# Kernel tuning notes

Hardware: AMD Instinct MI355X
Metric: run time of the kernel (lower is better)

## Reference

```python
import jax, jax.numpy as jnp
import numpy as np

N = 100_000          # nodes
E = 1_600_000        # edges
ORIG = 92            # orig_atom_fea_len
NBR = 41             # nbr_fea_len (RBF bins)
ATOM = 64            # atom_fea_len
NCONV = 3
H = 128              # h_fea_len
OUT = 1
NGRAPH = 256         # graphs in batch
ZDIM = 2 * ATOM + NBR  # CGConv concat dim = 169
RBF_VMIN, RBF_VMAX = 0.0, 8.0


def setup_inputs() -> dict:
    key = jax.random.key(0)
    ks = jax.random.split(key, 12)
    s = lambda fan: float(1.0 / np.sqrt(fan))
    u = lambda k, shape, fan: jax.random.uniform(k, shape, jnp.float32, -s(fan), s(fan))
    return {
        "x": jax.random.normal(ks[0], (N, ORIG), jnp.float32),
        "edge_attr": jax.random.normal(ks[1], (E, 3), jnp.float32),
        "W_emb": u(ks[2], (ORIG, ATOM), ORIG),
        "b_emb": u(ks[3], (ATOM,), ORIG),
        "Wf": u(ks[4], (NCONV, ZDIM, ATOM), ZDIM),
        "bf": u(ks[5], (NCONV, ATOM), ZDIM),
        "Ws": u(ks[6], (NCONV, ZDIM, ATOM), ZDIM),
        "bs": u(ks[7], (NCONV, ATOM), ZDIM),
        "bn_gamma": jnp.ones((NCONV, ATOM), jnp.float32),
        "bn_beta": jnp.zeros((NCONV, ATOM), jnp.float32),
        "W1": u(ks[8], (ATOM, H), ATOM),
        "b1": u(ks[9], (H,), ATOM),
        "W2": u(ks[10], (H, OUT), H),
        "b2": u(ks[11], (OUT,), H),
        "edge_index": jax.random.randint(jax.random.fold_in(key, 100), (2, E), 0, N),
        "batch": jnp.sort(jax.random.randint(jax.random.fold_in(key, 101), (N,), 0, NGRAPH)),
    }


def reference(x, edge_attr, W_emb, b_emb, Wf, bf, Ws, bs, bn_gamma, bn_beta,
              W1, b1, W2, b2, edge_index, batch):
    # atom embedding
    h = x @ W_emb + b_emb                                  # [N, ATOM]
    # edge distance -> RBF expansion (vmin=0, vmax=8, bins=NBR)
    d = jnp.sqrt(jnp.sum(edge_attr * edge_attr, axis=-1))  # [E]
    centers = jnp.linspace(RBF_VMIN, RBF_VMAX, NBR)
    gamma_rbf = 1.0 / ((RBF_VMAX - RBF_VMIN) / (NBR - 1))  # 1/lengthscale
    e = jnp.exp(-gamma_rbf * (d[:, None] - centers) ** 2)  # [E, NBR]

    src, dst = edge_index[0], edge_index[1]  # flow source->target: x_j = h[src], x_i = h[dst]
    for l in range(NCONV):
        # CGConv message: z = [x_i || x_j || e]; gate * core, scatter-add to i
        z = jnp.concatenate([h[dst], h[src], e], axis=-1)       # [E, ZDIM]
        msg = jax.nn.sigmoid(z @ Wf[l] + bf[l]) * jax.nn.softplus(z @ Ws[l] + bs[l])
        agg = jax.ops.segment_sum(msg, dst, num_segments=N)     # [N, ATOM]
        # BatchNorm (training-mode batch stats, eps=1e-5) then residual
        mu = agg.mean(axis=0)
        var = agg.var(axis=0)
        agg = bn_gamma[l] * (agg - mu) / jnp.sqrt(var + 1e-5) + bn_beta[l]
        h = jax.nn.softplus(agg + h)
    # global_add_pool over graphs, then MLP head
    g = jax.ops.segment_sum(h, batch, num_segments=NGRAPH)      # [NGRAPH, ATOM]
    out = jax.nn.softplus(g @ W1 + b1) @ W2 + b2                # [NGRAPH, OUT]
    return out
```

## Files before the change

kernel.cpp:

```cpp
#include <hip/hip_runtime.h>
#include <hip/hip_bf16.h>
#include <math.h>

#define N_NODES 100000
#define N_EDGES 1600000
#define ORIG    92
#define NBR     41
#define ATOM    64
#define NCONV   3
#define HFEA    128
#define NGRAPH  256
#define ZD      169
#define TBINS   5120
#define TMAX    10.0f
#define TS      ((TBINS + 1) * 64)
#define SP      72
#define SPE     136
#define NPBLK   128
#define LOG2E   1.4426950408889634f
#define LN2     0.6931471805599453f
#define NBKT    391
#define S1E     6250
#define S3CH    4096

typedef __attribute__((ext_vector_type(8))) short short8;
typedef __attribute__((ext_vector_type(4))) float f32x4;
typedef __attribute__((ext_vector_type(8))) int int8v;

__device__ __forceinline__ float softplus_f(float x) {
    return fmaxf(x, 0.0f) + log1pf(expf(-fabsf(x)));
}
__device__ __forceinline__ float sp_fast2(float x) {
    float t = x * LOG2E;
    return LN2 * (fmaxf(t, 0.0f) +
                  __builtin_amdgcn_logf(1.0f + __builtin_amdgcn_exp2f(-fabsf(t))));
}
__device__ __forceinline__ unsigned int pk_bf16(float lo, float hi) {
    unsigned int r;
    asm("v_cvt_pk_bf16_f32 %0, %1, %2" : "=v"(r) : "v"(lo), "v"(hi));
    return r;
}
__device__ __forceinline__ float bf_lo(unsigned int p) { return __uint_as_float(p << 16); }
__device__ __forceinline__ float bf_hi(unsigned int p) { return __uint_as_float(p & 0xffff0000u); }

__device__ __forceinline__ int lower_bound_i(const int* __restrict__ a, int n, int key) {
    int lo = 0, hi = n;
    while (lo < hi) {
        int mid = (lo + hi) >> 1;
        if (a[mid] < key) lo = mid + 1; else hi = mid;
    }
    return lo;
}

__global__ __launch_bounds__(256) void k_bhist(const int* __restrict__ ei,
                                               int* __restrict__ bucketCnt,
                                               int* __restrict__ flag,
                                               int* __restrict__ bucketBase,
                                               int* __restrict__ bucketCursor,
                                               int* __restrict__ offs) {
    __shared__ int cntL[NBKT];
    __shared__ int lastFlag;
    int tid = threadIdx.x;
    for (int i = tid; i < NBKT; i += 256) cntL[i] = 0;
    __syncthreads();
    int base = blockIdx.x * S1E;
    for (int i = tid; i < S1E; i += 256)
        atomicAdd(&cntL[ei[N_EDGES + base + i] >> 8], 1);
    __syncthreads();
    for (int i = tid; i < NBKT; i += 256)
        if (cntL[i]) atomicAdd(&bucketCnt[i], cntL[i]);
    if (tid == 0) {
        __threadfence();
        lastFlag = (atomicAdd(flag, 1) == 255) ? 1 : 0;
    }
    __syncthreads();
    if (lastFlag && tid < 64) {
        __threadfence();
        int carry = 0;
        for (int b0 = 0; b0 < NBKT; b0 += 64) {
            int idx = b0 + tid;
            int v0 = (idx < NBKT) ? bucketCnt[idx] : 0;
            int v = v0;
            for (int d = 1; d < 64; d <<= 1) {
                int u = __shfl_up(v, d, 64);
                if (tid >= d) v += u;
            }
            if (idx < NBKT) {
                int ex = carry + v - v0;
                bucketBase[idx] = ex;
                bucketCursor[idx] = ex;
            }
            carry += __shfl(v, 63, 64);
        }
        if (tid == 0) {
            bucketBase[NBKT] = N_EDGES;
            offs[N_NODES] = N_EDGES;
        }
    }
}

__global__ __launch_bounds__(256) void k_psort1(const int* __restrict__ ei,
                                                const float* __restrict__ ea,
                                                int* __restrict__ bucketCursor,
                                                int2* __restrict__ staging) {
    __shared__ int cntL[NBKT], scanB[NBKT], curL[NBKT], gbaseL[NBKT];
    __shared__ int sortedD[S3CH], sortedN[S3CH];
    int tid = threadIdx.x;
    int base = blockIdx.x * S3CH;
    int myCount = N_EDGES - base;
    if (myCount > S3CH) myCount = S3CH;
    for (int i = tid; i < NBKT; i += 256) { cntL[i] = 0; curL[i] = 0; }
    __syncthreads();
    int descr[16], dstr[16];
#pragma unroll
    for (int j = 0; j < 16; ++j) {
        int i = j * 256 + tid;
        descr[j] = 0; dstr[j] = -1;
        if (i < myCount) {
            int e = base + i;
            int src = ei[e];
            int dst = ei[N_EDGES + e];
            float a = ea[3 * e], bb = ea[3 * e + 1], c = ea[3 * e + 2];
            float d = sqrtf(a * a + bb * bb + c * c);
            int bin = (int)fminf(fmaf(d, (float)TBINS / TMAX, 0.5f), (float)TBINS);
            descr[j] = (bin << 17) | src;
            dstr[j] = dst;
            atomicAdd(&cntL[dst >> 8], 1);
        }
    }
    __syncthreads();
    if (tid < 64) {
        int carry = 0;
        for (int b0 = 0; b0 < NBKT; b0 += 64) {
            int idx = b0 + tid;
            int v0 = (idx < NBKT) ? cntL[idx] : 0;
            int v = v0;
            for (int d = 1; d < 64; d <<= 1) {
                int u = __shfl_up(v, d, 64);
                if (tid >= d) v += u;
            }
            if (idx < NBKT) scanB[idx] = carry + v - v0;
            carry += __shfl(v, 63, 64);
        }
    }
    __syncthreads();
#pragma unroll
    for (int j = 0; j < 16; ++j) {
        if (dstr[j] >= 0) {
            int b = dstr[j] >> 8;
            int pos = scanB[b] + atomicAdd(&curL[b], 1);
            sortedD[pos] = descr[j];
            sortedN[pos] = dstr[j];
        }
    }
    for (int i = tid; i < NBKT; i += 256)
        if (cntL[i] > 0) gbaseL[i] = atomicAdd(&bucketCursor[i], cntL[i]);
    __syncthreads();
    for (int i = tid; i < myCount; i += 256) {
        int n = sortedN[i];
        int b = n >> 8;
        int2 pr; pr.x = sortedD[i]; pr.y = n;
        staging[gbaseL[b] + (i - scanB[b])] = pr;
    }
}

__global__ __launch_bounds__(256) void k_psort2(const int* __restrict__ bucketBase,
                                                const int2* __restrict__ staging,
                                                int* __restrict__ edesc,
                                                int* __restrict__ offs) {
    __shared__ int cnt[256], sbase[256], cur[256];
    int b = blockIdx.x, tid = threadIdx.x;
    int base = bucketBase[b];
    int nb = bucketBase[b + 1] - base;
    cnt[tid] = 0; cur[tid] = 0;
    __syncthreads();
    for (int i = tid; i < nb; i += 256)
        atomicAdd(&cnt[staging[base + i].y & 255], 1);
    __syncthreads();
    int v = cnt[tid];
    sbase[tid] = v;
    __syncthreads();
    for (int d = 1; d < 256; d <<= 1) {
        int u = (tid >= d) ? sbase[tid - d] : 0;
        __syncthreads();
        sbase[tid] += u;
        __syncthreads();
    }
    int ex = sbase[tid] - v;
    int dst = (b << 8) + tid;
    if (dst < N_NODES) offs[dst] = base + ex;
    sbase[tid] = ex;
    __syncthreads();
    for (int i = tid; i < nb; i += 256) {
        int2 pr = staging[base + i];
        int local = pr.y & 255;
        int pos = base + sbase[local] + atomicAdd(&cur[local], 1);
        edesc[pos] = pr.x;
    }
}

__global__ __launch_bounds__(256) void k_table2(const float* __restrict__ Wf,
                                                const float* __restrict__ bf,
                                                const float* __restrict__ Ws,
                                                const float* __restrict__ bs,
                                                const float* __restrict__ We,
                                                unsigned int* __restrict__ Tp,
                                                unsigned int* __restrict__ Bp,
                                                unsigned int* __restrict__ BpE) {
    int tid = threadIdx.x;
    int l = blockIdx.y;
    if (blockIdx.x == 161) {
        int m = tid >> 6, c = tid & 63;
        const float* Wb = ((m & 2) ? Ws : Wf) + (size_t)l * ZD * ATOM + (m & 1) * ATOM * ATOM + c;
        unsigned int* dst = Bp + (size_t)l * 8192 + (size_t)tid * 32;
        for (int kp = 0; kp < 32; ++kp) {
            float w0 = Wb[(2 * kp) * ATOM] * LOG2E;
            float w1 = Wb[(2 * kp + 1) * ATOM] * LOG2E;
            dst[kp] = pk_bf16(w0, w1);
        }
        return;
    }
    if (blockIdx.x == 162) {
        if (l != 0) return;
        int n = tid & 63, q = tid >> 6;
        for (int kp = q * 16; kp < q * 16 + 16; ++kp) {
            int k0 = 2 * kp, k1 = 2 * kp + 1;
            float w0 = (k0 < ORIG) ? We[k0 * ATOM + n] : 0.f;
            float w1 = (k1 < ORIG) ? We[k1 * ATOM + n] : 0.f;
            BpE[(size_t)n * 64 + kp] = pk_bf16(w0, w1);
        }
        return;
    }
    __shared__ float Wc[NBR * 64], Wsc[NBR * 64], R[32 * NBR];
    int b0 = blockIdx.x * 32;
    const float* srcf = Wf + (size_t)l * ZD * ATOM + 2 * ATOM * ATOM;
    const float* srcs = Ws + (size_t)l * ZD * ATOM + 2 * ATOM * ATOM;
    for (int i = tid; i < NBR * 64; i += 256) {
        Wc[i] = srcf[i] * LOG2E;
        Wsc[i] = srcs[i] * LOG2E;
    }
    for (int i = tid; i < 32 * NBR; i += 256) {
        int bin = i / NBR, k = i - bin * NBR;
        float d = (b0 + bin) * (TMAX / TBINS);
        float diff = d - 0.2f * k;
        R[i] = expf(-5.0f * diff * diff);
    }
    __syncthreads();
    int c = tid & 63;
    float afb = bf[l * ATOM + c] * LOG2E, asb = bs[l * ATOM + c] * LOG2E;
#pragma unroll
    for (int it = 0; it < 8; ++it) {
        int bin = (tid >> 6) + 4 * it;
        int gb = b0 + bin;
        if (gb <= TBINS) {
            float af = afb, as = asb;
            for (int k = 0; k < NBR; ++k) {
                float r = R[bin * NBR + k];
                af += r * Wc[k * 64 + c];
                as += r * Wsc[k * 64 + c];
            }
            Tp[(size_t)l * TS + (size_t)gb * 64 + c] = pk_bf16(af, as);
        }
    }
}

__global__ __launch_bounds__(256) void k_embed_nodeP(const float* __restrict__ x,
                                                     const unsigned int* __restrict__ BpE,
                                                     const float* __restrict__ be,
                                                     const unsigned int* __restrict__ Bp,
                                                     float* __restrict__ h,
                                                     unsigned int* __restrict__ Pi,
                                                     unsigned int* __restrict__ Pj) {
    __shared__ char smem[46080];
    short* Ae = (short*)smem;
    short* Be = (short*)(smem + 17408);
    short* Bn = (short*)smem;
    short* An = (short*)(smem + 36864);
    int tid = threadIdx.x;
    int n0 = blockIdx.x * 64;
    for (int i = tid; i < 64 * 64; i += 256) {
        int r = i >> 6, kp = i & 63;
        int node = n0 + r;
        float2 v = make_float2(0.f, 0.f);
        if (node < N_NODES && kp < 46) v = ((const float2*)x)[(size_t)node * 46 + kp];
        *(unsigned int*)&Ae[r * SPE + kp * 2] = pk_bf16(v.x, v.y);
    }
    {
        const uint4* src = (const uint4*)BpE;
        for (int i = tid; i < 64 * 16; i += 256) {
            int row = i >> 4, q = i & 15;
            *(uint4*)&Be[row * SPE + q * 8] = src[i];
        }
    }
    __syncthreads();
    int lane = tid & 63, w = tid >> 6;
    int c15 = lane & 15, kb = lane >> 4;
    {
        short8 af[4];
#pragma unroll
        for (int s = 0; s < 4; ++s)
            af[s] = *(const short8*)&Ae[(16 * w + c15) * SPE + s * 32 + kb * 8];
        f32x4 acc[4];
#pragma unroll
        for (int t = 0; t < 4; ++t) acc[t] = (f32x4){0.f, 0.f, 0.f, 0.f};
#pragma unroll
        for (int t = 0; t < 4; ++t) {
#pragma unroll
            for (int s = 0; s < 4; ++s) {
                short8 bf8 = *(const short8*)&Be[(16 * t + c15) * SPE + s * 32 + kb * 8];
                acc[t] = __builtin_amdgcn_mfma_f32_16x16x32_bf16(af[s], bf8, acc[t], 0, 0, 0);
            }
        }
#pragma unroll
        for (int t = 0; t < 4; ++t) {
            float bias = be[16 * t + c15];
#pragma unroll
            for (int reg = 0; reg < 4; ++reg) {
                int row = 16 * w + kb * 4 + reg;
                int node = n0 + row;
                float v = acc[t][reg] + bias;
                if (node < N_NODES) h[(size_t)node * 64 + 16 * t + c15] = v;
                An[row * SP + 16 * t + c15] = (short)pk_bf16(v, v);
            }
        }
    }
    __syncthreads();
    {
        const uint4* src = (const uint4*)Bp;
        for (int i = tid; i < 2048; i += 256) {
            int row = i >> 3, j = i & 7;
            *(uint4*)&Bn[row * SP + j * 8] = src[row * 8 + j];
        }
    }
    __syncthreads();
    short8 af2[2];
#pragma unroll
    for (int s = 0; s < 2; ++s)
        af2[s] = *(const short8*)&An[(16 * w + c15) * SP + s * 32 + kb * 8];
    f32x4 acc2[16];
#pragma unroll
    for (int t = 0; t < 16; ++t) acc2[t] = (f32x4){0.f, 0.f, 0.f, 0.f};
#pragma unroll
    for (int t = 0; t < 16; ++t) {
#pragma unroll
        for (int s = 0; s < 2; ++s) {
            short8 bf8 = *(const short8*)&Bn[(16 * t + c15) * SP + s * 32 + kb * 8];
            acc2[t] = __builtin_amdgcn_mfma_f32_16x16x32_bf16(af2[s], bf8, acc2[t], 0, 0, 0);
        }
    }
#pragma unroll
    for (int t = 0; t < 4; ++t) {
#pragma unroll
        for (int reg = 0; reg < 4; ++reg) {
            int row = kb * 4 + reg;
            int node = n0 + 16 * w + row;
            if (node < N_NODES) {
                Pi[(size_t)node * 64 + 16 * t + c15] = pk_bf16(acc2[t][reg], acc2[t + 8][reg]);
                Pj[(size_t)node * 64 + 16 * t + c15] = pk_bf16(acc2[t + 4][reg], acc2[t + 12][reg]);
            }
        }
    }
}

__global__ __launch_bounds__(256) void k_nodeP_mfma(float* __restrict__ h,
                                                    const float* __restrict__ agg,
                                                    const float* __restrict__ ss,
                                                    const unsigned int* __restrict__ Bp,
                                                    int l,
                                                    unsigned int* __restrict__ Pi,
                                                    unsigned int* __restrict__ Pj) {
    __shared__ short A[64 * SP];
    __shared__ short B[256 * SP];
    int tid = threadIdx.x;
    int n0 = blockIdx.x * 64;
    for (int i = tid; i < 64 * 32; i += 256) {
        int r = i >> 5, kp = i & 31;
        int node = n0 + r;
        int gi = node * 32 + kp;
        float2 hv = make_float2(0.f, 0.f);
        if (node < N_NODES) {
            hv = ((const float2*)h)[gi];
            float2 av = ((const float2*)agg)[gi];
            int c = kp * 2;
            float x0 = ss[c] * av.x + ss[64 + c] + hv.x;
            float x1 = ss[c + 1] * av.y + ss[64 + c + 1] + hv.y;
            hv.x = sp_fast2(x0);
            hv.y = sp_fast2(x1);
            ((float2*)h)[gi] = hv;
        }
        *(unsigned int*)&A[r * SP + kp * 2] = pk_bf16(hv.x, hv.y);
    }
    {
        const uint4* src = (const uint4*)(Bp + (size_t)l * 8192);
        for (int i = tid; i < 2048; i += 256) {
            int row = i >> 3, j = i & 7;
            *(uint4*)&B[row * SP + j * 8] = src[row * 8 + j];
        }
    }
    __syncthreads();
    int lane = tid & 63, w = tid >> 6;
    int c15 = lane & 15, kb = lane >> 4;
    short8 af[2];
#pragma unroll
    for (int s = 0; s < 2; ++s)
        af[s] = *(const short8*)&A[(16 * w + c15) * SP + s * 32 + kb * 8];
    f32x4 acc[16];
#pragma unroll
    for (int t = 0; t < 16; ++t) acc[t] = (f32x4){0.f, 0.f, 0.f, 0.f};
#pragma unroll
    for (int t = 0; t < 16; ++t) {
#pragma unroll
        for (int s = 0; s < 2; ++s) {
            short8 bf8 = *(const short8*)&B[(16 * t + c15) * SP + s * 32 + kb * 8];
            acc[t] = __builtin_amdgcn_mfma_f32_16x16x32_bf16(af[s], bf8, acc[t], 0, 0, 0);
        }
    }
#pragma unroll
    for (int t = 0; t < 4; ++t) {
#pragma unroll
        for (int reg = 0; reg < 4; ++reg) {
            int row = kb * 4 + reg;
            int node = n0 + 16 * w + row;
            if (node < N_NODES) {
                Pi[(size_t)node * 64 + 16 * t + c15] = pk_bf16(acc[t][reg], acc[t + 8][reg]);
                Pj[(size_t)node * 64 + 16 * t + c15] = pk_bf16(acc[t + 4][reg], acc[t + 12][reg]);
            }
        }
    }
}

__global__ __launch_bounds__(256, 4) void k_edge_sorted(const int* __restrict__ offs,
                                                        const int* __restrict__ edesc,
                                                        const unsigned int* __restrict__ Pi,
                                                        const unsigned int* __restrict__ Pj,
                                                        const unsigned int* __restrict__ Tp,
                                                        float* __restrict__ agg) {
    int wid = (blockIdx.x * 256 + threadIdx.x) >> 6;
    int lane = threadIdx.x & 63;
    if (wid >= N_NODES) return;
    int uwid = __builtin_amdgcn_readfirstlane(wid);
    int2 kk;
    asm volatile("s_load_dwordx2 %0, %1, 0x0\n\ts_waitcnt lgkmcnt(0)"
                 : "=s"(kk) : "s"(offs + uwid));
    int ko = kk.x, ke = kk.y;
    unsigned int pi = Pi[(size_t)uwid * 64 + lane];
    float gi = bf_lo(pi), ci = bf_hi(pi);
    float acc = 0.0f;
    int lane4 = lane * 4;
    const char* PjB = (const char*)Pj;
    const char* TpB = (const char*)Tp;
    int k0 = ko;
    for (; k0 + 16 <= ke; k0 += 16) {
        int8v e0, e1;
        asm volatile(
            "s_load_dwordx8 %0, %2, 0x0\n\t"
            "s_load_dwordx8 %1, %2, 0x20\n\t"
            "s_waitcnt lgkmcnt(0)"
            : "=&s"(e0), "=&s"(e1)
            : "s"(edesc + k0));
        unsigned int pjv[16], tjv[16];
#pragma unroll
        for (int j = 0; j < 16; ++j) {
            int v = (j < 8) ? e0[j & 7] : e1[j & 7];
            int sb = (v & 0x1FFFF) << 8;
            int tb = (v >> 17) << 8;
            pjv[j] = *(const unsigned int*)(PjB + sb + lane4);
            tjv[j] = *(const unsigned int*)(TpB + tb + lane4);
        }
#pragma unroll
        for (int j = 0; j < 16; ++j) {
            float g = gi + bf_lo(pjv[j]) + bf_lo(tjv[j]);
            float c = ci + bf_hi(pjv[j]) + bf_hi(tjv[j]);
            float sg = __builtin_amdgcn_rcpf(1.0f + __builtin_amdgcn_exp2f(-g));
            float sp = fmaxf(c, 0.0f) + __builtin_amdgcn_logf(1.0f + __builtin_amdgcn_exp2f(-fabsf(c)));
            acc = fmaf(sg, sp, acc);
        }
    }
    if (k0 < ke) {
        int8v e0, e1;
        asm volatile(
            "s_load_dwordx8 %0, %2, 0x0\n\t"
            "s_load_dwordx8 %1, %2, 0x20\n\t"
            "s_waitcnt lgkmcnt(0)"
            : "=&s"(e0), "=&s"(e1)
            : "s"(edesc + k0));
        unsigned int pjv[16], tjv[16];
#pragma unroll
        for (int j = 0; j < 16; ++j) {
            if (k0 + j < ke) {
                int v = (j < 8) ? e0[j & 7] : e1[j & 7];
                int sb = (v & 0x1FFFF) << 8;
                int tb = (v >> 17) << 8;
                pjv[j] = *(const unsigned int*)(PjB + sb + lane4);
                tjv[j] = *(const unsigned int*)(TpB + tb + lane4);
            }
        }
#pragma unroll
        for (int j = 0; j < 16; ++j) {
            if (k0 + j < ke) {
                float g = gi + bf_lo(pjv[j]) + bf_lo(tjv[j]);
                float c = ci + bf_hi(pjv[j]) + bf_hi(tjv[j]);
                float sg = __builtin_amdgcn_rcpf(1.0f + __builtin_amdgcn_exp2f(-g));
                float sp = fmaxf(c, 0.0f) + __builtin_amdgcn_logf(1.0f + __builtin_amdgcn_exp2f(-fabsf(c)));
                acc = fmaf(sg, sp, acc);
            }
        }
    }
    agg[(size_t)uwid * 64 + lane] = acc * LN2;
}

__global__ __launch_bounds__(256) void k_bnstats2(const float* __restrict__ agg,
                                                  float* __restrict__ partial,
                                                  int* __restrict__ lcnt,
                                                  const float* __restrict__ gamma,
                                                  const float* __restrict__ beta,
                                                  int l, float* __restrict__ ss) {
    __shared__ f32x4 ls4[256], ls24[256];
    __shared__ float ls[128];
    __shared__ int lastFlag;
    int tid = threadIdx.x;
    const f32x4* agg4 = (const f32x4*)agg;
    f32x4 s = (f32x4){0.f, 0.f, 0.f, 0.f};
    f32x4 s2 = (f32x4){0.f, 0.f, 0.f, 0.f};
    for (int i = blockIdx.x * 256 + tid; i < N_NODES * 16; i += NPBLK * 256) {
        f32x4 v = agg4[i];
        s += v;
        s2 += v * v;
    }
    ls4[tid] = s; ls24[tid] = s2;
    __syncthreads();
    for (int d = 128; d >= 16; d >>= 1) {
        if (tid < d) { ls4[tid] += ls4[tid + d]; ls24[tid] += ls24[tid + d]; }
        __syncthreads();
    }
    if (tid < 16) {
#pragma unroll
        for (int j = 0; j < 4; ++j) {
            partial[blockIdx.x * 128 + tid * 4 + j] = ls4[tid][j];
            partial[blockIdx.x * 128 + 64 + tid * 4 + j] = ls24[tid][j];
        }
    }
    __syncthreads();
    if (tid == 0) {
        __threadfence();
        lastFlag = (atomicAdd(lcnt, 1) == NPBLK - 1) ? 1 : 0;
    }
    __syncthreads();
    if (lastFlag) {
        __threadfence();
        if (tid < 128) {
            float sum = 0.0f;
            for (int b = 0; b < NPBLK; ++b) sum += partial[b * 128 + tid];
            ls[tid] = sum;
        }
        __syncthreads();
        if (tid < 64) {
            const float inv = 1.0f / (float)N_NODES;
            float mu = ls[tid] * inv;
            float var = ls[64 + tid] * inv - mu * mu;
            float sc = gamma[l * ATOM + tid] * rsqrtf(var + 1e-5f);
            ss[tid] = sc;
            ss[64 + tid] = beta[l * ATOM + tid] - mu * sc;
        }
    }
}

__global__ __launch_bounds__(128) void k_head2(const float* __restrict__ agg,
                                               const float* __restrict__ ss,
                                               const float* __restrict__ h,
                                               const int* __restrict__ batch,
                                               const float* __restrict__ W1,
                                               const float* __restrict__ b1,
                                               const float* __restrict__ W2,
                                               const float* __restrict__ b2,
                                               float* __restrict__ out) {
    __shared__ float gvec[64];
    __shared__ float red[128];
    int gid = blockIdx.x, tid = threadIdx.x;
    int lo = lower_bound_i(batch, N_NODES, gid);
    int hi = lower_bound_i(batch, N_NODES, gid + 1);
    int c = tid & 63, half = tid >> 6;
    float sc = ss[c], sh = ss[64 + c];
    float acc = 0.0f;
    for (int n = lo + half; n < hi; n += 2) {
        float xv = sc * agg[(size_t)n * 64 + c] + sh + h[(size_t)n * 64 + c];
        acc += sp_fast2(xv);
    }
    red[tid] = acc;
    __syncthreads();
    if (tid < 64) gvec[tid] = red[tid] + red[tid + 64];
    __syncthreads();
    float a2 = b1[tid];
    for (int k = 0; k < ATOM; ++k) a2 += gvec[k] * W1[k * HFEA + tid];
    red[tid] = softplus_f(a2) * W2[tid];
    __syncthreads();
    for (int s = 64; s > 0; s >>= 1) {
        if (tid < s) red[tid] += red[tid + s];
        __syncthreads();
    }
    if (tid == 0) out[gid] = red[0] + b2[0];
}

extern "C" void kernel_launch(void* const* d_in, const int* in_sizes, int n_in,
                              void* d_out, int out_size, void* d_ws, size_t ws_size,
                              hipStream_t stream) {
    const float* x       = (const float*)d_in[0];
    const float* ea      = (const float*)d_in[1];
    const float* W_emb   = (const float*)d_in[2];
    const float* b_emb   = (const float*)d_in[3];
    const float* Wf      = (const float*)d_in[4];
    const float* bf      = (const float*)d_in[5];
    const float* Ws      = (const float*)d_in[6];
    const float* bs      = (const float*)d_in[7];
    const float* bn_g    = (const float*)d_in[8];
    const float* bn_b    = (const float*)d_in[9];
    const float* W1      = (const float*)d_in[10];
    const float* b1      = (const float*)d_in[11];
    const float* W2      = (const float*)d_in[12];
    const float* b2      = (const float*)d_in[13];
    const int*   ei      = (const int*)d_in[14];
    const int*   batch   = (const int*)d_in[15];
    float* out = (float*)d_out;

    char* wsb = (char*)d_ws;
    size_t off = 0;
    auto alloc = [&](size_t bytes) { char* p = wsb + off; off += (bytes + 255) & ~(size_t)255; return p; };
    float*        h        = (float*)alloc((size_t)N_NODES * 64 * 4);
    float*        agg      = (float*)alloc((size_t)N_NODES * 64 * 4);
    unsigned int* Pi       = (unsigned int*)alloc((size_t)N_NODES * 64 * 4);
    unsigned int* Pj       = (unsigned int*)alloc((size_t)N_NODES * 64 * 4);
    int*          edesc    = (int*)alloc((size_t)(N_EDGES + 16) * 4);
    int2*         staging  = (int2*)alloc((size_t)N_EDGES * 8);
    int*          meta     = (int*)alloc(1024 * 4);
    int*          bucketCnt    = meta;
    int*          lcnt         = meta + 512;
    int*          bucketBase   = (int*)alloc(520 * 4);
    int*          bucketCursor = (int*)alloc(512 * 4);
    int*          offs     = (int*)alloc((size_t)(N_NODES + 1) * 4);
    unsigned int* Tp       = (unsigned int*)alloc((size_t)NCONV * TS * 4);
    unsigned int* Bp       = (unsigned int*)alloc((size_t)NCONV * 8192 * 4);
    unsigned int* BpE      = (unsigned int*)alloc((size_t)64 * 64 * 4);
    float*        partial  = (float*)alloc((size_t)NPBLK * 128 * 4);
    float*        ss       = (float*)alloc(128 * 4);

    (void)hipMemsetAsync(meta, 0, 1024 * 4, stream);
    k_bhist<<<256, 256, 0, stream>>>(ei, bucketCnt, lcnt + 3, bucketBase, bucketCursor, offs);
    k_psort1<<<(N_EDGES + S3CH - 1) / S3CH, 256, 0, stream>>>(ei, ea, bucketCursor, staging);
    k_psort2<<<NBKT, 256, 0, stream>>>(bucketBase, staging, edesc, offs);

    dim3 tg(163, NCONV);
    k_table2<<<tg, 256, 0, stream>>>(Wf, bf, Ws, bs, W_emb, Tp, Bp, BpE);
    k_embed_nodeP<<<(N_NODES + 63) / 64, 256, 0, stream>>>(x, BpE, b_emb, Bp, h, Pi, Pj);

    for (int l = 0; l < NCONV; ++l) {
        if (l > 0)
            k_nodeP_mfma<<<(N_NODES + 63) / 64, 256, 0, stream>>>(h, agg, ss, Bp, l, Pi, Pj);
        k_edge_sorted<<<(N_NODES * 64 + 255) / 256, 256, 0, stream>>>(
            offs, edesc, Pi, Pj, Tp + (size_t)l * TS, agg);
        k_bnstats2<<<NPBLK, 256, 0, stream>>>(agg, partial, lcnt + l, bn_g, bn_b, l, ss);
    }

    k_head2<<<NGRAPH, 128, 0, stream>>>(agg, ss, h, batch, W1, b1, W2, b2, out);
}
```

Baseline: 501.5 us.

## Split pooling into node-parallel atomic pool kernel and separate MLP head

Global add pooling used to run as one block per graph (256 blocks), each binary-searching the sorted batch array and looping over about 390 nodes with 128 threads. It is now a node-parallel kernel of about 1563 blocks in which each wavefront covers 16 consecutive nodes, keeps a running sum per graph and flushes it with atomicAdd whenever the graph id changes. A small separate head kernel then runs the MLP. The goal is better GPU occupancy for the final pooling pass, at the cost of an extra memset, an extra launch and float atomics, which make the summation order nondeterministic.

```diff
diff --git a/kernel.cpp b/kernel.cpp
--- a/kernel.cpp
+++ b/kernel.cpp
@@ -42,15 +42,6 @@
 }
 __device__ __forceinline__ float bf_lo(unsigned int p) { return __uint_as_float(p << 16); }
 __device__ __forceinline__ float bf_hi(unsigned int p) { return __uint_as_float(p & 0xffff0000u); }
-
-__device__ __forceinline__ int lower_bound_i(const int* __restrict__ a, int n, int key) {
-    int lo = 0, hi = n;
-    while (lo < hi) {
-        int mid = (lo + hi) >> 1;
-        if (a[mid] < key) lo = mid + 1; else hi = mid;
-    }
-    return lo;
-}
 
 __global__ __launch_bounds__(256) void k_bhist(const int* __restrict__ ei,
                                                int* __restrict__ bucketCnt,
@@ -565,40 +556,48 @@
     }
 }
 
-__global__ __launch_bounds__(128) void k_head2(const float* __restrict__ agg,
+__global__ __launch_bounds__(256) void k_pool2(const float* __restrict__ agg,
                                                const float* __restrict__ ss,
                                                const float* __restrict__ h,
                                                const int* __restrict__ batch,
-                                               const float* __restrict__ W1,
-                                               const float* __restrict__ b1,
-                                               const float* __restrict__ W2,
-                                               const float* __restrict__ b2,
-                                               float* __restrict__ out) {
-    __shared__ float gvec[64];
+                                               float* __restrict__ g) {
+    int w = threadIdx.x >> 6, lane = threadIdx.x & 63;
+    int nbase = blockIdx.x * 64 + w * 16;
+    float acc = 0.0f;
+    int curg = -1;
+    float sc = ss[lane], sh = ss[64 + lane];
+    for (int i = 0; i < 16; ++i) {
+        int n = nbase + i;
+        if (n >= N_NODES) break;
+        int gid = __builtin_amdgcn_readfirstlane(batch[n]);
+        if (gid != curg) {
+            if (curg >= 0) atomicAdd(&g[(size_t)curg * ATOM + lane], acc);
+            curg = gid;
+            acc = 0.0f;
+        }
+        float x = sc * agg[(size_t)n * 64 + lane] + sh + h[(size_t)n * 64 + lane];
+        acc += sp_fast2(x);
+    }
+    if (curg >= 0) atomicAdd(&g[(size_t)curg * ATOM + lane], acc);
+}
+
+__global__ __launch_bounds__(128) void k_head(const float* __restrict__ g,
+                                              const float* __restrict__ W1,
+                                              const float* __restrict__ b1,
+                                              const float* __restrict__ W2,
+                                              const float* __restrict__ b2,
+                                              float* __restrict__ out) {
     __shared__ float red[128];
-    int gid = blockIdx.x, tid = threadIdx.x;
-    int lo = lower_bound_i(batch, N_NODES, gid);
-    int hi = lower_bound_i(batch, N_NODES, gid + 1);
-    int c = tid & 63, half = tid >> 6;
-    float sc = ss[c], sh = ss[64 + c];
-    float acc = 0.0f;
-    for (int n = lo + half; n < hi; n += 2) {
-        float xv = sc * agg[(size_t)n * 64 + c] + sh + h[(size_t)n * 64 + c];
-        acc += sp_fast2(xv);
-    }
-    red[tid] = acc;
-    __syncthreads();
-    if (tid < 64) gvec[tid] = red[tid] + red[tid + 64];
-    __syncthreads();
-    float a2 = b1[tid];
-    for (int k = 0; k < ATOM; ++k) a2 += gvec[k] * W1[k * HFEA + tid];
-    red[tid] = softplus_f(a2) * W2[tid];
+    int gid = blockIdx.x, j = threadIdx.x;
+    float acc = b1[j];
+    for (int k = 0; k < ATOM; ++k) acc += g[gid * ATOM + k] * W1[k * HFEA + j];
+    red[j] = softplus_f(acc) * W2[j];
     __syncthreads();
     for (int s = 64; s > 0; s >>= 1) {
-        if (tid < s) red[tid] += red[tid + s];
+        if (j < s) red[j] += red[j + s];
         __syncthreads();
     }
-    if (tid == 0) out[gid] = red[0] + b2[0];
+    if (j == 0) out[gid] = red[0] + b2[0];
 }
 
 extern "C" void kernel_launch(void* const* d_in, const int* in_sizes, int n_in,
@@ -642,6 +641,7 @@
     unsigned int* BpE      = (unsigned int*)alloc((size_t)64 * 64 * 4);
     float*        partial  = (float*)alloc((size_t)NPBLK * 128 * 4);
     float*        ss       = (float*)alloc(128 * 4);
+    float*        g        = (float*)alloc((size_t)NGRAPH * 64 * 4);
 
     (void)hipMemsetAsync(meta, 0, 1024 * 4, stream);
     k_bhist<<<256, 256, 0, stream>>>(ei, bucketCnt, lcnt + 3, bucketBase, bucketCursor, offs);
@@ -660,5 +660,7 @@
         k_bnstats2<<<NPBLK, 256, 0, stream>>>(agg, partial, lcnt + l, bn_g, bn_b, l, ss);
     }
 
-    k_head2<<<NGRAPH, 128, 0, stream>>>(agg, ss, h, batch, W1, b1, W2, b2, out);
-}
+    (void)hipMemsetAsync(g, 0, (size_t)NGRAPH * 64 * 4, stream);
+    k_pool2<<<(N_NODES + 63) / 64, 256, 0, stream>>>(agg, ss, h, batch, g);
+    k_head<<<NGRAPH, 128, 0, stream>>>(g, W1, b1, W2, b2, out);
+}
```

Result: faster. 445.4 us (-11.2%).
